# Optimization experiments

Measured on AMD Instinct MI355X. Metric: run time of the kernel, lower is better.

## Reference

```python
import jax, jax.numpy as jnp
import numpy as np

E_LAMBDA = 1e-4


def _conv1d(x, w, b=None, pad=0):
    # x: (C, L) unbatched, w: (O, I, K)
    y = jax.lax.conv_general_dilated(
        x[None], w, window_strides=(1,), padding=[(pad, pad)],
        dimension_numbers=("NCH", "OIH", "NCH"))[0]
    if b is not None:
        y = y + b[:, None]
    return y


def _avg_pool2(x):
    # kernel 2 stride 2 along last axis; x: (C, L) -> (C, L//2)
    C, L = x.shape
    return x.reshape(C, L // 2, 2).mean(axis=-1)


def _simam(x):
    # x: (C, L); torch version runs on (1, C, L) so stats are global
    n = x.shape[0] * x.shape[1] - 1
    d = (x - x.mean()) ** 2
    y = d / (4.0 * (d.sum() / n + E_LAMBDA)) + 0.5
    return x + x * jax.nn.sigmoid(y)


def setup_inputs() -> dict:
    key = jax.random.key(0)
    ks = jax.random.split(key, 6)
    C, L = 2048, 4096  # L must equal 2*C for Tiss broadcast to be valid
    inp = jax.random.normal(ks[0], (C, L), dtype=jnp.float32)
    insum = jax.random.normal(ks[1], (C, L), dtype=jnp.float32)
    conv1_w = jax.random.normal(ks[2], (C, C, 3), dtype=jnp.float32) * (1.0 / np.sqrt(3 * C))
    fc_w = jax.random.normal(ks[3], (C, C, 1), dtype=jnp.float32) * (1.0 / np.sqrt(C))
    fc_b = jax.random.normal(ks[4], (C,), dtype=jnp.float32) * 0.01
    mix_w = jnp.array([-0.8], dtype=jnp.float32)
    return {"input": inp, "insum": insum, "conv1_w": conv1_w,
            "fc_w": fc_w, "fc_b": fc_b, "mix_w": mix_w}


def reference(input, insum, conv1_w, fc_w, fc_b, mix_w):
    x = _avg_pool2(input)        # (C, L/2)
    x_mfcc = _avg_pool2(insum)   # (C, L/2)

    input_new = _simam(input)
    insum_new = _simam(insum)

    x1 = _conv1d(x, conv1_w, pad=1)          # (C, L/2)
    x_mfcc1 = _conv1d(x_mfcc, conv1_w, pad=1)
    x2 = _conv1d(x, fc_w, fc_b, pad=0).T      # (L/2, C)
    x_mfcc2 = _conv1d(x_mfcc1, fc_w, fc_b, pad=0).T  # (L/2, C)

    out1 = jax.nn.sigmoid((x1 @ x_mfcc2).sum(axis=1))          # (C,)
    out2 = jax.nn.sigmoid((x_mfcc1.T @ x2.T).sum(axis=1))      # (L/2,) == (C,)

    mf = jax.nn.sigmoid(mix_w)                                  # (1,)
    out = out1 * mf + out2 * (1.0 - mf)                         # (C,)

    out = jax.nn.sigmoid(_conv1d(out[:, None], conv1_w, pad=1))  # (C, 1)

    input_insum = input_new * 0.6 + insum_new * 0.4             # (C, L)
    return input_insum * out
```

## Files before the change

### kernel.cpp

```cpp
#include <hip/hip_runtime.h>
#include <math.h>

#define C  2048
#define L  4096
#define L2 2048
#define CW3 6144

constexpr size_t OFF_RS_A = 0;
constexpr size_t OFF_RQ_A = 2048;
constexpr size_t OFF_RS_B = 4096;
constexpr size_t OFF_RQ_B = 6144;
constexpr size_t OFF_SCAL = 8192;
constexpr size_t OFF_CW   = 8208;
constexpr size_t OFF_G    = 10256;
constexpr size_t OFF_H    = 16400;
constexpr size_t OFF_V    = 22544;
constexpr size_t OFF_O2   = 24592;
constexpr size_t OFF_S    = 26640;
constexpr size_t OFF_U    = 28688;
constexpr size_t OFF_MIX  = 34832;

constexpr size_t PA_OFF = 0;
constexpr size_t PB_OFF = 4194304;

__device__ __forceinline__ float wredf(float v) {
#pragma unroll
  for (int o = 32; o; o >>= 1) v += __shfl_down(v, o, 64);
  return v;
}
__device__ __forceinline__ double wredd(double v) {
#pragma unroll
  for (int o = 32; o; o >>= 1) v += __shfl_down(v, o, 64);
  return v;
}
__device__ __forceinline__ float sigm(float x) { return 1.f / (1.f + expf(-x)); }
__device__ __forceinline__ float simam1(float x, float m, float cf) {
  float d = x - m;
  float y = d * d * cf + 0.5f;
  return x * (1.f + 1.f / (1.f + expf(-y)));
}

__global__ void w1(const float* __restrict__ A, const float* __restrict__ B,
                   const float* __restrict__ fc_w, float* __restrict__ ws,
                   float* __restrict__ dout) {
  int u = blockIdx.x;
  int tid = threadIdx.x;
  if (u < 4096) {
    __shared__ float sm[8];
    const float* src = (u < 2048) ? A : B;
    int row = u & 2047;
    const float4* p = (const float4*)(src + (size_t)row * L);
    float2* pool = (float2*)(dout + ((u < 2048) ? PA_OFF : PB_OFF) + (size_t)row * L2);
    float s = 0.f, q = 0.f;
#pragma unroll
    for (int i = tid; i < L / 4; i += 256) {
      float4 v = p[i];
      s += (v.x + v.y) + (v.z + v.w);
      q += (v.x * v.x + v.y * v.y) + (v.z * v.z + v.w * v.w);
      float2 pm;
      pm.x = (v.x + v.y) * 0.5f;
      pm.y = (v.z + v.w) * 0.5f;
      pool[i] = pm;
    }
    s = wredf(s); q = wredf(q);
    int lane = tid & 63, wv = tid >> 6;
    if (!lane) { sm[wv] = s; sm[4 + wv] = q; }
    __syncthreads();
    if (!tid) {
      float* rs = ws + ((u < 2048) ? OFF_RS_A : OFF_RS_B);
      float* rq = ws + ((u < 2048) ? OFF_RQ_A : OFF_RQ_B);
      rs[row] = sm[0] + sm[1] + sm[2] + sm[3];
      rq[row] = sm[4] + sm[5] + sm[6] + sm[7];
    }
  } else {
    int cb = u - 4096;
    int rg = cb >> 3;
    int col = (cb & 7) * 256 + tid;
    const float* p = fc_w + (size_t)rg * 64 * C + col;
    float acc = 0.f;
#pragma unroll 8
    for (int k = 0; k < 64; ++k) acc += p[(size_t)k * C];
    atomicAdd(ws + OFF_CW + col, acc);
  }
}

__global__ void w2(const float* __restrict__ fc_w, const float* __restrict__ fc_b,
                   float* __restrict__ ws) {
  int u = blockIdx.x;
  int tid = threadIdx.x;
  int lane = tid & 63, wv = tid >> 6;
  if (u < 2048) {
    __shared__ float sl[4];
    const float4* w = (const float4*)(fc_w + (size_t)u * C);
    const float4* rx = (const float4*)(ws + OFF_RS_A);
    float acc = 0.f;
#pragma unroll
    for (int i = tid; i < C / 4; i += 256) {
      float4 a = w[i], r = rx[i];
      acc += a.x * r.x + a.y * r.y + a.z * r.z + a.w * r.w;
    }
    acc = wredf(acc);
    if (!lane) sl[wv] = acc;
    __syncthreads();
    if (!tid)
      (ws + OFF_S)[u] = 0.5f * (sl[0] + sl[1] + sl[2] + sl[3]) + (float)L2 * fc_b[u];
  } else {
    __shared__ double sd[5];
    const float* arr = ws + (wv == 0 ? OFF_RS_A : wv == 1 ? OFF_RQ_A
                                                          : wv == 2 ? OFF_RS_B : OFF_RQ_B);
    double acc = 0.0, accb = 0.0;
    for (int i = lane; i < 2048; i += 64) {
      acc += (double)arr[i];
      if (wv == 0) accb += (double)fc_b[i];
    }
    acc = wredd(acc);
    if (wv == 0) accb = wredd(accb);
    if (!lane) { sd[wv] = acc; if (wv == 0) sd[4] = accb; }
    __syncthreads();
    if (!tid) {
      const double N = (double)C * (double)L, n = N - 1.0;
      double dA = sd[1] - sd[0] * sd[0] / N;
      double dB = sd[3] - sd[2] * sd[2] / N;
      float* s = ws + OFF_SCAL;
      s[0] = (float)(sd[0] / N);
      s[1] = (float)(1.0 / (4.0 * (dA / n + 1e-4)));
      s[2] = (float)(sd[2] / N);
      s[3] = (float)(1.0 / (4.0 * (dB / n + 1e-4)));
      s[4] = (float)sd[4];
    }
  }
}

__global__ void w3(const float* __restrict__ conv1_w, float* __restrict__ ws) {
  __shared__ float lcw[64], ls[64];
  int u = blockIdx.x;
  int tid = threadIdx.x;
  int cc = u % 24, rg = u / 24;
  int col = cc * 256 + tid;
  int i0 = rg * 64;
  if (tid < 64) {
    lcw[tid] = (ws + OFF_CW)[i0 + tid];
    ls[tid] = (ws + OFF_S)[i0 + tid];
  }
  __syncthreads();
  const float* base = conv1_w + (size_t)i0 * CW3 + col;
  float ag = 0.f, ah = 0.f;
#pragma unroll 8
  for (int k = 0; k < 64; ++k) {
    float wv = base[(size_t)k * CW3];
    ag += lcw[k] * wv;
    ah += ls[k] * wv;
  }
  atomicAdd(ws + OFF_G + col, ag);
  atomicAdd(ws + OFF_H + col, ah);
}

__global__ void w4(const float* __restrict__ dout, float* __restrict__ ws) {
  __shared__ float gsh[48], hsh[48];
  int u = blockIdx.x;
  int tid = threadIdx.x;
  int kb = u & 7, cg = u >> 3;
  int c0 = cg * 16;
  int k = kb * 256 + tid;
  if (tid < 48) gsh[tid] = (ws + OFF_G)[c0 * 3 + tid];
  else if (tid >= 64 && tid < 112) hsh[tid - 64] = (ws + OFF_H)[c0 * 3 + tid - 64];
  __syncthreads();
  float accv = 0.f, acco = 0.f;
#pragma unroll
  for (int c = 0; c < 16; ++c) {
    const float* row = dout + PB_OFF + (size_t)(c0 + c) * L2;
    float xc = row[k];
    float xl = (k > 0) ? row[k - 1] : 0.f;
    float xr = (k < L2 - 1) ? row[k + 1] : 0.f;
    accv += gsh[c * 3] * xl + gsh[c * 3 + 1] * xc + gsh[c * 3 + 2] * xr;
    acco += hsh[c * 3] * xl + hsh[c * 3 + 1] * xc + hsh[c * 3 + 2] * xr;
  }
  atomicAdd(ws + OFF_V + k, accv);
  atomicAdd(ws + OFF_O2 + k, acco);
}

__global__ void w5(const float* __restrict__ dout, float* __restrict__ ws) {
  __shared__ float vsh[2050];
  __shared__ float s12[12];
  int u = blockIdx.x;
  int tid = threadIdx.x;
  float sb = (ws + OFF_SCAL)[4];
  if (tid == 0) { vsh[0] = 0.f; vsh[2049] = 0.f; }
  for (int j = tid; j < L2; j += 256) vsh[1 + j] = (ws + OFF_V)[j] + sb;
  __syncthreads();
  const float* prow = dout + PA_OFF + (size_t)u * L2;
  float a0 = 0.f, a1 = 0.f, a2 = 0.f;
#pragma unroll
  for (int j = tid; j < L2; j += 256) {
    float xm = prow[j];
    a0 += xm * vsh[j + 2];
    a1 += xm * vsh[j + 1];
    a2 += xm * vsh[j];
  }
  a0 = wredf(a0); a1 = wredf(a1); a2 = wredf(a2);
  int lane = tid & 63, wv = tid >> 6;
  if (!lane) { s12[wv] = a0; s12[4 + wv] = a1; s12[8 + wv] = a2; }
  __syncthreads();
  if (!tid) {
    (ws + OFF_U)[u * 3 + 0] = s12[0] + s12[1] + s12[2] + s12[3];
    (ws + OFF_U)[u * 3 + 1] = s12[4] + s12[5] + s12[6] + s12[7];
    (ws + OFF_U)[u * 3 + 2] = s12[8] + s12[9] + s12[10] + s12[11];
  }
}

__global__ void w6(const float* __restrict__ conv1_w, const float* __restrict__ mix_w,
                   float* __restrict__ ws) {
  __shared__ float sl[4];
  int u = blockIdx.x;
  int tid = threadIdx.x;
  const float4* w4p = (const float4*)(conv1_w + (size_t)u * CW3);
  const float4* u4 = (const float4*)(ws + OFF_U);
  float acc = 0.f;
#pragma unroll
  for (int m = tid; m < CW3 / 4; m += 256) {
    float4 wv = w4p[m], uv = u4[m];
    acc += wv.x * uv.x + wv.y * uv.y + wv.z * uv.z + wv.w * uv.w;
  }
  acc = wredf(acc);
  int lane = tid & 63, wv = tid >> 6;
  if (!lane) sl[wv] = acc;
  __syncthreads();
  if (!tid) {
    float mfv = sigm(mix_w[0]);
    float o1 = sigm(sl[0] + sl[1] + sl[2] + sl[3]);
    float o2 = sigm((ws + OFF_O2)[u]);
    (ws + OFF_MIX)[u] = o1 * mfv + o2 * (1.f - mfv);
  }
}

__global__ void w7(const float* __restrict__ input, const float* __restrict__ insum,
                   const float* __restrict__ conv1_w, float* __restrict__ out,
                   const float* __restrict__ ws) {
  __shared__ float sl[4];
  __shared__ float shov;
  int u = blockIdx.x;
  int tid = threadIdx.x;
  const float4* w4p = (const float4*)(conv1_w + (size_t)u * CW3);
  const float4* m4 = (const float4*)(ws + OFF_MIX);
  float acc = 0.f;
#pragma unroll
  for (int p = tid; p < 512; p += 256) {
    float4 f0 = w4p[3 * p], f1 = w4p[3 * p + 1], f2 = w4p[3 * p + 2];
    float4 m = m4[p];
    acc += f0.y * m.x + f1.x * m.y + f1.w * m.z + f2.z * m.w;
  }
  acc = wredf(acc);
  int lane = tid & 63, wv = tid >> 6;
  if (!lane) sl[wv] = acc;
  __syncthreads();
  if (!tid) shov = sigm(sl[0] + sl[1] + sl[2] + sl[3]);
  __syncthreads();
  float ovc = shov;
  const float* scal = ws + OFF_SCAL;
  float mA = scal[0], cA = scal[1], mB = scal[2], cB = scal[3];
  size_t base = (size_t)u * L;
  const float4* pa = (const float4*)(input + base);
  const float4* pb = (const float4*)(insum + base);
  float4* po = (float4*)(out + base);
#pragma unroll
  for (int i = tid; i < L / 4; i += 256) {
    float4 a = pa[i], b = pb[i], r;
    r.x = (simam1(a.x, mA, cA) * 0.6f + simam1(b.x, mB, cB) * 0.4f) * ovc;
    r.y = (simam1(a.y, mA, cA) * 0.6f + simam1(b.y, mB, cB) * 0.4f) * ovc;
    r.z = (simam1(a.z, mA, cA) * 0.6f + simam1(b.z, mB, cB) * 0.4f) * ovc;
    r.w = (simam1(a.w, mA, cA) * 0.6f + simam1(b.w, mB, cB) * 0.4f) * ovc;
    po[i] = r;
  }
}

extern "C" void kernel_launch(void* const* d_in, const int* in_sizes, int n_in,
                              void* d_out, int out_size, void* d_ws, size_t ws_size,
                              hipStream_t stream) {
  const float* input   = (const float*)d_in[0];
  const float* insum   = (const float*)d_in[1];
  const float* conv1_w = (const float*)d_in[2];
  const float* fc_w    = (const float*)d_in[3];
  const float* fc_b    = (const float*)d_in[4];
  const float* mix_w   = (const float*)d_in[5];
  float* out = (float*)d_out;
  float* ws  = (float*)d_ws;

  hipMemsetAsync((char*)d_ws + OFF_CW * 4, 0, 18432 * 4, stream);

  dim3 b(256);
  w1<<<4352, b, 0, stream>>>(input, insum, fc_w, ws, out);
  w2<<<2049, b, 0, stream>>>(fc_w, fc_b, ws);
  w3<<<768, b, 0, stream>>>(conv1_w, ws);
  w4<<<1024, b, 0, stream>>>(out, ws);
  w5<<<2048, b, 0, stream>>>(out, ws);
  w6<<<2048, b, 0, stream>>>(conv1_w, mix_w, ws);
  w7<<<2048, b, 0, stream>>>(input, insum, conv1_w, out, ws);
}
```

Before: 235.6 us.

## Drop pooled intermediates, recompute pooling on the fly, replace atomics with partial sums

Stops writing the avg-pooled copies of input and insum to scratch in w1. w4 and w5 now recompute the pooling directly from the original tensors. The atomicAdd accumulations (CW, G, H, V, O2) become per-slice partial buffers in the output buffer, reduced by the consumer kernels, which also removes the memset. w4 now uses 128 blocks of 128 channels each, which cuts parallelism and may leave that kernel latency-bound.

```diff
diff --git a/kernel.cpp b/kernel.cpp
--- a/kernel.cpp
+++ b/kernel.cpp
@@ -11,17 +11,15 @@
 constexpr size_t OFF_RS_B = 4096;
 constexpr size_t OFF_RQ_B = 6144;
 constexpr size_t OFF_SCAL = 8192;
-constexpr size_t OFF_CW   = 8208;
-constexpr size_t OFF_G    = 10256;
-constexpr size_t OFF_H    = 16400;
-constexpr size_t OFF_V    = 22544;
-constexpr size_t OFF_O2   = 24592;
-constexpr size_t OFF_S    = 26640;
-constexpr size_t OFF_U    = 28688;
-constexpr size_t OFF_MIX  = 34832;
-
-constexpr size_t PA_OFF = 0;
-constexpr size_t PB_OFF = 4194304;
+constexpr size_t OFF_S    = 8208;
+constexpr size_t OFF_U    = 10256;
+constexpr size_t OFF_MIX  = 16400;
+
+constexpr size_t SC_CWP  = 0;
+constexpr size_t SC_GP   = 65536;
+constexpr size_t SC_HP   = 262144;
+constexpr size_t SC_VP   = 458752;
+constexpr size_t SC_O2P  = 491520;
 
 __device__ __forceinline__ float wredf(float v) {
 #pragma unroll
@@ -42,7 +40,7 @@
 
 __global__ void w1(const float* __restrict__ A, const float* __restrict__ B,
                    const float* __restrict__ fc_w, float* __restrict__ ws,
-                   float* __restrict__ dout) {
+                   float* __restrict__ sc) {
   int u = blockIdx.x;
   int tid = threadIdx.x;
   if (u < 4096) {
@@ -50,17 +48,12 @@
     const float* src = (u < 2048) ? A : B;
     int row = u & 2047;
     const float4* p = (const float4*)(src + (size_t)row * L);
-    float2* pool = (float2*)(dout + ((u < 2048) ? PA_OFF : PB_OFF) + (size_t)row * L2);
     float s = 0.f, q = 0.f;
 #pragma unroll
     for (int i = tid; i < L / 4; i += 256) {
       float4 v = p[i];
       s += (v.x + v.y) + (v.z + v.w);
       q += (v.x * v.x + v.y * v.y) + (v.z * v.z + v.w * v.w);
-      float2 pm;
-      pm.x = (v.x + v.y) * 0.5f;
-      pm.y = (v.z + v.w) * 0.5f;
-      pool[i] = pm;
     }
     s = wredf(s); q = wredf(q);
     int lane = tid & 63, wv = tid >> 6;
@@ -80,7 +73,7 @@
     float acc = 0.f;
 #pragma unroll 8
     for (int k = 0; k < 64; ++k) acc += p[(size_t)k * C];
-    atomicAdd(ws + OFF_CW + col, acc);
+    (sc + SC_CWP)[(size_t)rg * C + col] = acc;
   }
 }
 
@@ -131,7 +124,8 @@
   }
 }
 
-__global__ void w3(const float* __restrict__ conv1_w, float* __restrict__ ws) {
+__global__ void w3(const float* __restrict__ conv1_w, const float* __restrict__ ws,
+                   float* __restrict__ sc) {
   __shared__ float lcw[64], ls[64];
   int u = blockIdx.x;
   int tid = threadIdx.x;
@@ -139,7 +133,10 @@
   int col = cc * 256 + tid;
   int i0 = rg * 64;
   if (tid < 64) {
-    lcw[tid] = (ws + OFF_CW)[i0 + tid];
+    float a = 0.f;
+#pragma unroll 8
+    for (int p = 0; p < 32; ++p) a += (sc + SC_CWP)[(size_t)p * C + i0 + tid];
+    lcw[tid] = a;
     ls[tid] = (ws + OFF_S)[i0 + tid];
   }
   __syncthreads();
@@ -151,48 +148,70 @@
     ag += lcw[k] * wv;
     ah += ls[k] * wv;
   }
-  atomicAdd(ws + OFF_G + col, ag);
-  atomicAdd(ws + OFF_H + col, ah);
-}
-
-__global__ void w4(const float* __restrict__ dout, float* __restrict__ ws) {
-  __shared__ float gsh[48], hsh[48];
+  (sc + SC_GP)[(size_t)rg * CW3 + col] = ag;
+  (sc + SC_HP)[(size_t)rg * CW3 + col] = ah;
+}
+
+__global__ void w4(const float* __restrict__ insum, float* __restrict__ sc) {
+  __shared__ float gsh[384], hsh[384];
   int u = blockIdx.x;
   int tid = threadIdx.x;
   int kb = u & 7, cg = u >> 3;
-  int c0 = cg * 16;
+  int c0 = cg * 128;
   int k = kb * 256 + tid;
-  if (tid < 48) gsh[tid] = (ws + OFF_G)[c0 * 3 + tid];
-  else if (tid >= 64 && tid < 112) hsh[tid - 64] = (ws + OFF_H)[c0 * 3 + tid - 64];
+  for (int idx = tid; idx < 384; idx += 256) {
+    float ag = 0.f, ah = 0.f;
+#pragma unroll 8
+    for (int p = 0; p < 32; ++p) {
+      ag += (sc + SC_GP)[(size_t)p * CW3 + c0 * 3 + idx];
+      ah += (sc + SC_HP)[(size_t)p * CW3 + c0 * 3 + idx];
+    }
+    gsh[idx] = ag;
+    hsh[idx] = ah;
+  }
   __syncthreads();
   float accv = 0.f, acco = 0.f;
-#pragma unroll
-  for (int c = 0; c < 16; ++c) {
-    const float* row = dout + PB_OFF + (size_t)(c0 + c) * L2;
-    float xc = row[k];
-    float xl = (k > 0) ? row[k - 1] : 0.f;
-    float xr = (k < L2 - 1) ? row[k + 1] : 0.f;
+  for (int c = 0; c < 128; ++c) {
+    const float* row = insum + (size_t)(c0 + c) * L;
+    float2 bm = *(const float2*)(row + 2 * k);
+    float xc = (bm.x + bm.y) * 0.5f;
+    float xl = 0.f, xr = 0.f;
+    if (k > 0) {
+      float2 am = *(const float2*)(row + 2 * k - 2);
+      xl = (am.x + am.y) * 0.5f;
+    }
+    if (k < L2 - 1) {
+      float2 dm = *(const float2*)(row + 2 * k + 2);
+      xr = (dm.x + dm.y) * 0.5f;
+    }
     accv += gsh[c * 3] * xl + gsh[c * 3 + 1] * xc + gsh[c * 3 + 2] * xr;
     acco += hsh[c * 3] * xl + hsh[c * 3 + 1] * xc + hsh[c * 3 + 2] * xr;
   }
-  atomicAdd(ws + OFF_V + k, accv);
-  atomicAdd(ws + OFF_O2 + k, acco);
-}
-
-__global__ void w5(const float* __restrict__ dout, float* __restrict__ ws) {
+  (sc + SC_VP)[(size_t)cg * L2 + k] = accv;
+  (sc + SC_O2P)[(size_t)cg * L2 + k] = acco;
+}
+
+__global__ void w5(const float* __restrict__ input, const float* __restrict__ sc,
+                   float* __restrict__ ws) {
   __shared__ float vsh[2050];
   __shared__ float s12[12];
   int u = blockIdx.x;
   int tid = threadIdx.x;
   float sb = (ws + OFF_SCAL)[4];
   if (tid == 0) { vsh[0] = 0.f; vsh[2049] = 0.f; }
-  for (int j = tid; j < L2; j += 256) vsh[1 + j] = (ws + OFF_V)[j] + sb;
-  __syncthreads();
-  const float* prow = dout + PA_OFF + (size_t)u * L2;
+  for (int j = tid; j < L2; j += 256) {
+    float a = sb;
+#pragma unroll 8
+    for (int sl = 0; sl < 16; ++sl) a += (sc + SC_VP)[(size_t)sl * L2 + j];
+    vsh[1 + j] = a;
+  }
+  __syncthreads();
+  const float* row = input + (size_t)u * L;
   float a0 = 0.f, a1 = 0.f, a2 = 0.f;
 #pragma unroll
   for (int j = tid; j < L2; j += 256) {
-    float xm = prow[j];
+    float2 ab = *(const float2*)(row + 2 * j);
+    float xm = (ab.x + ab.y) * 0.5f;
     a0 += xm * vsh[j + 2];
     a1 += xm * vsh[j + 1];
     a2 += xm * vsh[j];
@@ -209,7 +228,7 @@
 }
 
 __global__ void w6(const float* __restrict__ conv1_w, const float* __restrict__ mix_w,
-                   float* __restrict__ ws) {
+                   const float* __restrict__ sc, float* __restrict__ ws) {
   __shared__ float sl[4];
   int u = blockIdx.x;
   int tid = threadIdx.x;
@@ -226,9 +245,12 @@
   if (!lane) sl[wv] = acc;
   __syncthreads();
   if (!tid) {
+    float o2r = 0.f;
+#pragma unroll 8
+    for (int slc = 0; slc < 16; ++slc) o2r += (sc + SC_O2P)[(size_t)slc * L2 + u];
     float mfv = sigm(mix_w[0]);
     float o1 = sigm(sl[0] + sl[1] + sl[2] + sl[3]);
-    float o2 = sigm((ws + OFF_O2)[u]);
+    float o2 = sigm(o2r);
     (ws + OFF_MIX)[u] = o1 * mfv + o2 * (1.f - mfv);
   }
 }
@@ -284,15 +306,14 @@
   const float* mix_w   = (const float*)d_in[5];
   float* out = (float*)d_out;
   float* ws  = (float*)d_ws;
-
-  hipMemsetAsync((char*)d_ws + OFF_CW * 4, 0, 18432 * 4, stream);
+  float* sc  = out;
 
   dim3 b(256);
-  w1<<<4352, b, 0, stream>>>(input, insum, fc_w, ws, out);
+  w1<<<4352, b, 0, stream>>>(input, insum, fc_w, ws, sc);
   w2<<<2049, b, 0, stream>>>(fc_w, fc_b, ws);
-  w3<<<768, b, 0, stream>>>(conv1_w, ws);
-  w4<<<1024, b, 0, stream>>>(out, ws);
-  w5<<<2048, b, 0, stream>>>(out, ws);
-  w6<<<2048, b, 0, stream>>>(conv1_w, mix_w, ws);
+  w3<<<768, b, 0, stream>>>(conv1_w, ws, sc);
+  w4<<<128, b, 0, stream>>>(insum, sc);
+  w5<<<2048, b, 0, stream>>>(input, sc, ws);
+  w6<<<2048, b, 0, stream>>>(conv1_w, mix_w, sc, ws);
   w7<<<2048, b, 0, stream>>>(input, insum, conv1_w, out, ws);
 }
```

After: 324.2 us. 37.6% more time.
